# Kernel tuning notes

Hardware: AMD Instinct MI355X
Metric: run time of the kernel (lower is better)

The kernel has to match this reference:

```python
import jax, jax.numpy as jnp
import numpy as np

C = 64           # channels
CPG = 8          # channel_per_group
G = C // CPG     # offset groups = 8
K = 27           # 3x3x3 taps
N, D, H, W = 2, 8, 56, 56


def conv3d(x, w, b=None):
    y = jax.lax.conv_general_dilated(
        x, w, window_strides=(1, 1, 1), padding=[(1, 1)] * 3,
        dimension_numbers=('NCDHW', 'OIDHW', 'NCDHW'))
    if b is not None:
        y = y + b.reshape(1, -1, 1, 1, 1)
    return y


def deform_conv3d(x, off, w, groups):
    # x: [N,C,D,H,W]; off: [N, G*3*27, D,H,W]; w: [O,C,3,3,3]
    n, cin, d, h, wd = x.shape
    cpg = cin // groups
    p = d * h * wd
    off = off.reshape(n, groups, K, 3, d, h, wd)
    # kernel tap displacements in (kd,kh,kw) order, each in {-1,0,1}
    r = jnp.arange(3, dtype=x.dtype) - 1.0
    taps = jnp.stack(jnp.meshgrid(r, r, r, indexing='ij'), axis=-1).reshape(K, 3)
    gd = jnp.arange(d, dtype=x.dtype)[:, None, None]
    gh = jnp.arange(h, dtype=x.dtype)[None, :, None]
    gw = jnp.arange(wd, dtype=x.dtype)[None, None, :]
    # sampling positions [N,G,K,D,H,W]
    pd = gd + taps[:, 0][:, None, None, None] + off[:, :, :, 0]
    ph = gh + taps[:, 1][:, None, None, None] + off[:, :, :, 1]
    pw = gw + taps[:, 2][:, None, None, None] + off[:, :, :, 2]
    d0 = jnp.floor(pd); h0 = jnp.floor(ph); w0 = jnp.floor(pw)
    fd, fh, fw = pd - d0, ph - h0, pw - w0
    d0 = d0.astype(jnp.int32); h0 = h0.astype(jnp.int32); w0 = w0.astype(jnp.int32)
    xflat = x.reshape(n, groups, cpg, p)[:, :, None]  # [N,G,1,Cpg,P]
    acc = jnp.zeros((n, groups, K, cpg, p), x.dtype)
    for cd in (0, 1):
        for ch in (0, 1):
            for cw in (0, 1):
                idd, idh, idw = d0 + cd, h0 + ch, w0 + cw
                wgt = ((fd if cd else 1.0 - fd)
                       * (fh if ch else 1.0 - fh)
                       * (fw if cw else 1.0 - fw))
                valid = ((idd >= 0) & (idd < d) & (idh >= 0) & (idh < h)
                         & (idw >= 0) & (idw < wd)).astype(x.dtype)
                lin = ((jnp.clip(idd, 0, d - 1) * h + jnp.clip(idh, 0, h - 1)) * wd
                       + jnp.clip(idw, 0, wd - 1))
                g = jnp.take_along_axis(xflat, lin.reshape(n, groups, K, 1, p), axis=-1)
                acc = acc + g * (wgt * valid).reshape(n, groups, K, 1, p)
    # [N,G,K,Cpg,P] -> [N,K,C,P]
    vals = acc.transpose(0, 2, 1, 3, 4).reshape(n, K, cin, p)
    out = jnp.einsum('oik,nkip->nop', w.reshape(w.shape[0], cin, K), vals)
    return out.reshape(n, -1, d, h, wd)


def batchnorm(x, gamma, beta, eps=1e-5):
    m = x.mean((0, 2, 3, 4), keepdims=True)
    v = x.var((0, 2, 3, 4), keepdims=True)
    return (gamma.reshape(1, -1, 1, 1, 1) * (x - m) * jax.lax.rsqrt(v + eps)
            + beta.reshape(1, -1, 1, 1, 1))


def setup_inputs() -> dict:
    key = jax.random.key(0)
    ks = jax.random.split(key, 4)
    fan = C * K
    x = jax.random.normal(ks[0], (N, C, D, H, W), jnp.float32)
    w_off = jax.random.normal(ks[1], (G * 3 * K, C, 3, 3, 3), jnp.float32) * 0.01
    b_off = jnp.zeros((G * 3 * K,), jnp.float32)
    w1 = jax.random.normal(ks[2], (C, C, 3, 3, 3), jnp.float32) / np.sqrt(fan).astype(np.float32)
    w2 = jax.random.normal(ks[3], (C, C, 3, 3, 3), jnp.float32) / np.sqrt(fan).astype(np.float32)
    return dict(x=x, w_off=w_off, b_off=b_off, w1=w1,
                gamma1=jnp.ones((C,), jnp.float32), beta1=jnp.zeros((C,), jnp.float32),
                w2=w2, b2=jnp.zeros((C,), jnp.float32),
                gamma2=jnp.ones((C,), jnp.float32), beta2=jnp.zeros((C,), jnp.float32))


def reference(x, w_off, b_off, w1, gamma1, beta1, w2, b2, gamma2, beta2):
    residual = x
    off = conv3d(x, w_off, b_off)
    out = deform_conv3d(x, off, w1, G)
    out = jax.nn.relu(batchnorm(out, gamma1, beta1))
    out = conv3d(out, w2, b2)
    out = batchnorm(out, gamma2, beta2) + residual
    return jax.nn.relu(out)
```

## Files before the change

### kernel.cpp

```cpp
#include <hip/hip_runtime.h>
#include <hip/hip_bf16.h>

#define N_ 2
#define C_ 64
#define D_ 8
#define H_ 56
#define W_ 56
#define HW_ (H_*W_)
#define P_ (D_*HW_)
#define G_ 8
#define CPG_ 8
#define K_ 27
#define CO_OFF_ 648
#define MP_ 768
#define KK_ 1728
#define KB_ (KK_*2)

typedef __attribute__((ext_vector_type(8))) short shortx8;
typedef __attribute__((ext_vector_type(4))) float floatx4;
#define AS1 __attribute__((address_space(1)))
#define AS3 __attribute__((address_space(3)))

__device__ inline float b2f(unsigned short u) {
    union { unsigned u; float f; } x; x.u = ((unsigned)u) << 16; return x.f;
}
__device__ inline unsigned short f2b(float f) {
    union { float f; unsigned u; } x; x.f = f;
    unsigned r = (x.u + 0x7fffu + ((x.u >> 16) & 1u)) >> 16;
    return (unsigned short)r;
}
__device__ inline float lof(unsigned u) { union { unsigned u; float f; } x; x.u = u << 16; return x.f; }
__device__ inline float hif(unsigned u) { union { unsigned u; float f; } x; x.u = u & 0xffff0000u; return x.f; }


__global__ __launch_bounds__(256) void transpose_xt_kernel(
    const float* __restrict__ x, unsigned short* __restrict__ xt)
{
    __shared__ unsigned short tile[64][65];
    int b  = blockIdx.x;
    int n  = b / (P_/64);
    int p0 = (b % (P_/64))*64;
    int tid = threadIdx.x;
    int j  = tid & 63;
    int c0 = (tid >> 6)*16;
    for (int r = 0; r < 16; ++r)
        tile[c0 + r][j] = f2b(x[((size_t)n*C_ + c0 + r)*P_ + p0 + j]);
    __syncthreads();
    unsigned* dst = (unsigned*)(xt + ((size_t)n*P_ + p0)*C_);
    #pragma unroll
    for (int it = 0; it < 8; ++it) {
        int wi  = it*256 + tid;
        int row = wi >> 5;
        int c   = (wi & 31)*2;
        unsigned lo = tile[c][row], hi = tile[c+1][row];
        dst[(size_t)row*32 + (wi & 31)] = lo | (hi << 16);
    }
}

__global__ __launch_bounds__(256) void permA1k_kernel(
    const float* __restrict__ w, unsigned short* __restrict__ A)
{
    int i = blockIdx.x*256 + threadIdx.x;
    if (i >= MP_*KK_) return;
    int m = i / KK_, r = i % KK_;
    int kk = r / 64, ci = r % 64;
    A[i] = (m < CO_OFF_) ? f2b(w[((size_t)m*C_ + ci)*K_ + kk]) : (unsigned short)0;
}

__global__ __launch_bounds__(256) void perm_w_kernel(
    const float* __restrict__ w, unsigned short* __restrict__ At)
{
    int tid = blockIdx.x*256 + threadIdx.x;
    if (tid >= C_*KK_) return;
    int o  = tid / KK_;
    int r  = tid % KK_;
    int k  = r / 64, i = r % 64;
    At[tid] = f2b(w[((size_t)o*C_ + i)*K_ + k]);
}

__global__ __launch_bounds__(256) void conv_off_fused(
    const unsigned short* __restrict__ A,
    const unsigned short* __restrict__ xt,
    const float* __restrict__ bias,
    unsigned short* __restrict__ off2)
{
    __shared__ __align__(16) short As[2][16*512];
    __shared__ __align__(16) short Bs[16*512];
    int tid = threadIdx.x;
    int w = tid >> 6, lane = tid & 63;
    int n   = blockIdx.x / 980;
    int bid = blockIdx.x % 980;
    int mt, nt;
    if (bid < 960) { int c = bid/40, r = bid%40; mt = r >> 3; nt = c*8 + (r&7); }
    else           { int r = bid - 960;          mt = r >> 2; nt = 192 + (r&3); }
    int m0 = mt*128, p0 = nt*128;
    int lm = lane & 15, lq = lane >> 4;

    const unsigned short* xtn = xt + (size_t)n*P_*C_;
    unsigned short* out2 = off2 + (size_t)n*216*P_*3;

    const char* Ab0 = (const char*)A + (size_t)(m0 + w*32 + lm)*KB_ + lq*16;
    const char* Ab1 = Ab0 + (size_t)16*KB_;

    int oct = lane & 7;
    int prj[4], dj[4], hj[4], wj[4];
    #pragma unroll
    for (int j = 0; j < 4; ++j) {
        int prow = j*32 + w*8 + (lane >> 3);
        prj[j] = prow;
        int p = p0 + prow;
        dj[j] = p / HW_;
        int hw2 = p % HW_;
        hj[j] = hw2 / W_;
        wj[j] = hw2 % W_;
    }

    auto stageA = [&](int kt, int buf) {
        __builtin_amdgcn_global_load_lds((const AS1 unsigned*)(Ab0 + kt*128),      (AS3 unsigned*)(&As[buf][(w*2)*512]),     16, 0, 0);
        __builtin_amdgcn_global_load_lds((const AS1 unsigned*)(Ab1 + kt*128),      (AS3 unsigned*)(&As[buf][(w*2+1)*512]),   16, 0, 0);
        __builtin_amdgcn_global_load_lds((const AS1 unsigned*)(Ab0 + kt*128 + 64), (AS3 unsigned*)(&As[buf][(8+w*2)*512]),   16, 0, 0);
        __builtin_amdgcn_global_load_lds((const AS1 unsigned*)(Ab1 + kt*128 + 64), (AS3 unsigned*)(&As[buf][(8+w*2+1)*512]), 16, 0, 0);
    };
    auto loadB = [&](int kt, uint4* B) {
        int kd = kt/9 - 1, kh = (kt/3)%3 - 1, kw = kt%3 - 1;
        int delta = kd*HW_ + kh*W_ + kw;
        #pragma unroll
        for (int j = 0; j < 4; ++j) {
            bool v = ((unsigned)(dj[j]+kd) < (unsigned)D_) &&
                     ((unsigned)(hj[j]+kh) < (unsigned)H_) &&
                     ((unsigned)(wj[j]+kw) < (unsigned)W_);
            uint4 val = {0u,0u,0u,0u};
            if (v) val = *(const uint4*)(xtn + (size_t)(p0 + prj[j] + delta)*C_ + oct*8);
            B[j] = val;
        }
    };

    int mh = w >> 1, nh = w & 1;
    floatx4 acc[4][4];
    #pragma unroll
    for (int i = 0; i < 4; ++i)
        #pragma unroll
        for (int j = 0; j < 4; ++j)
            acc[i][j] = (floatx4){0.f, 0.f, 0.f, 0.f};

    uint4 Bcur[4], Bnext[4];
    #pragma unroll
    for (int j = 0; j < 4; ++j) Bnext[j] = (uint4){0u,0u,0u,0u};
    stageA(0, 0);
    loadB(0, Bcur);

    for (int kt = 0; kt < 27; ++kt) {
        int buf = kt & 1;
        __syncthreads();
        #pragma unroll
        for (int j = 0; j < 4; ++j) {
            int chunk = (oct>>2)*8 + (prj[j]>>4);
            *(uint4*)&Bs[chunk*512 + ((oct&3)*16 + ((prj[j]&15) ^ oct))*8] = Bcur[j];
        }
        __syncthreads();
        if (kt < 26) { stageA(kt+1, buf^1); loadB(kt+1, Bnext); }
        #pragma unroll
        for (int ks = 0; ks < 2; ++ks) {
            int swzB = (lq*16 + (lm ^ (ks*4 + lq)))*8;
            shortx8 a[4], b[4];
            #pragma unroll
            for (int i = 0; i < 4; ++i) a[i] = *(const shortx8*)&As[buf][(ks*8 + 4*mh + i)*512 + lane*8];
            #pragma unroll
            for (int j = 0; j < 4; ++j) b[j] = *(const shortx8*)&Bs[(ks*8 + 4*nh + j)*512 + swzB];
            #pragma unroll
            for (int i = 0; i < 4; ++i)
                #pragma unroll
                for (int j = 0; j < 4; ++j)
                    acc[i][j] = __builtin_amdgcn_mfma_f32_16x16x32_bf16(a[i], b[j], acc[i][j], 0, 0, 0);
        }
        #pragma unroll
        for (int j = 0; j < 4; ++j) Bcur[j] = Bnext[j];
    }

    #pragma unroll
    for (int i = 0; i < 4; ++i) {
        int cob = m0 + (4*mh+i)*16 + lq*4;
        #pragma unroll
        for (int r = 0; r < 4; ++r) {
            int co = cob + r;
            float bv = bias[co];
            int row2 = co / 3, comp = co % 3;
            size_t base = (size_t)row2*P_*3 + comp;
            #pragma unroll
            for (int j = 0; j < 4; ++j) {
                int col = p0 + (4*nh+j)*16 + lm;
                out2[base + (size_t)col*3] = f2b(acc[i][j][r] + bv);
            }
        }
    }
}

__global__ __launch_bounds__(256) void conv_off_tail(
    const unsigned short* __restrict__ A,
    const unsigned short* __restrict__ xt,
    const float* __restrict__ bias,
    unsigned short* __restrict__ off2)
{
    __shared__ __align__(16) short As[54*512];
    __shared__ __align__(16) short Bs[16*512];
    int tid = threadIdx.x;
    int w = tid >> 6, lane = tid & 63;
    int n  = blockIdx.x / 196;
    int p0 = (blockIdx.x % 196)*128;
    int lm = lane & 15, lq = lane >> 4;

    const unsigned short* xtn = xt + (size_t)n*P_*C_;
    unsigned short* out2 = off2 + (size_t)n*216*P_*3;

    const char* Abase = (const char*)A + (size_t)(640 + lm)*KB_ + lq*16;
    for (int ch = w; ch < 54; ch += 4)
        __builtin_amdgcn_global_load_lds((const AS1 unsigned*)(Abase + ch*64),
                                         (AS3 unsigned*)(As + ch*512), 16, 0, 0);

    int oct = lane & 7;
    int prj[4], dj[4], hj[4], wj[4];
    #pragma unroll
    for (int j = 0; j < 4; ++j) {
        int prow = j*32 + w*8 + (lane >> 3);
        prj[j] = prow;
        int p = p0 + prow;
        dj[j] = p / HW_;
        int hw2 = p % HW_;
        hj[j] = hw2 / W_;
        wj[j] = hw2 % W_;
    }
    auto loadB = [&](int kt, uint4* B) {
        int kd = kt/9 - 1, kh = (kt/3)%3 - 1, kw = kt%3 - 1;
        int delta = kd*HW_ + kh*W_ + kw;
        #pragma unroll
        for (int j = 0; j < 4; ++j) {
            bool v = ((unsigned)(dj[j]+kd) < (unsigned)D_) &&
                     ((unsigned)(hj[j]+kh) < (unsigned)H_) &&
                     ((unsigned)(wj[j]+kw) < (unsigned)W_);
            uint4 val = {0u,0u,0u,0u};
            if (v) val = *(const uint4*)(xtn + (size_t)(p0 + prj[j] + delta)*C_ + oct*8);
            B[j] = val;
        }
    };

    floatx4 acc[2];
    acc[0] = (floatx4){0.f,0.f,0.f,0.f};
    acc[1] = (floatx4){0.f,0.f,0.f,0.f};

    uint4 Bcur[4], Bnext[4];
    #pragma unroll
    for (int j = 0; j < 4; ++j) Bnext[j] = (uint4){0u,0u,0u,0u};
    loadB(0, Bcur);

    for (int kt = 0; kt < 27; ++kt) {
        __syncthreads();
        #pragma unroll
        for (int j = 0; j < 4; ++j) {
            int chunk = (oct>>2)*8 + (prj[j]>>4);
            *(uint4*)&Bs[chunk*512 + ((oct&3)*16 + ((prj[j]&15) ^ oct))*8] = Bcur[j];
        }
        __syncthreads();
        if (kt < 26) loadB(kt+1, Bnext);
        #pragma unroll
        for (int ks = 0; ks < 2; ++ks) {
            int swzB = (lq*16 + (lm ^ (ks*4 + lq)))*8;
            shortx8 a = *(const shortx8*)&As[(kt*2 + ks)*512 + lane*8];
            #pragma unroll
            for (int j = 0; j < 2; ++j) {
                shortx8 b = *(const shortx8*)&Bs[(ks*8 + w*2 + j)*512 + swzB];
                acc[j] = __builtin_amdgcn_mfma_f32_16x16x32_bf16(a, b, acc[j], 0, 0, 0);
            }
        }
        #pragma unroll
        for (int j = 0; j < 4; ++j) Bcur[j] = Bnext[j];
    }

    #pragma unroll
    for (int j = 0; j < 2; ++j) {
        #pragma unroll
        for (int r = 0; r < 4; ++r) {
            int co = 640 + lq*4 + r;
            if (co < CO_OFF_) {
                int col = p0 + w*32 + j*16 + lm;
                out2[((size_t)(co/3)*P_ + col)*3 + (co%3)] = f2b(acc[j][r] + bias[co]);
            }
        }
    }
}

__global__ __launch_bounds__(256) void deform_fused(
    const unsigned short* __restrict__ xt,
    const unsigned short* __restrict__ off2,
    const unsigned short* __restrict__ A,
    unsigned short* __restrict__ y1t)
{
    __shared__ __align__(16) short SH[12288];
    int tid = threadIdx.x;
    int w = tid >> 6, lane = tid & 63;
    int n  = blockIdx.x / (P_/32);
    int p0 = (blockIdx.x % (P_/32))*32;
    int lm = lane & 15, lq = lane >> 4;

    const unsigned short* offn = off2 + (size_t)n*216*P_*3;
    const uint4* xg0 = (const uint4*)(xt + (size_t)n*P_*C_);

    const char* Ab = (const char*)A + (size_t)(w*16 + lm)*KB_ + lq*16;

    int g = lane & 7;
    int prow = tid >> 3;
    int p = p0 + prow;
    int dd = p / HW_;
    int hw2 = p % HW_;
    int hh = hw2 / W_;
    int ww = hw2 % W_;
    int bchunk = (g>>2)*2 + (prow>>4);
    int boffs  = ((g&3)*16 + ((prow&15) ^ g))*8;

    auto stageA = [&](int kt, int buf) {
        __builtin_amdgcn_global_load_lds((const AS1 unsigned*)(Ab + kt*128),      (AS3 unsigned*)(SH + buf*4096 + w*512),     16, 0, 0);
        __builtin_amdgcn_global_load_lds((const AS1 unsigned*)(Ab + kt*128 + 64), (AS3 unsigned*)(SH + buf*4096 + (4+w)*512), 16, 0, 0);
    };
    auto loadOff = [&](int kt, float* o) {
        size_t idx = ((size_t)(g*K_ + kt)*P_ + p)*3;
        o[0] = b2f(offn[idx]);
        o[1] = b2f(offn[idx + 1]);
        o[2] = b2f(offn[idx + 2]);
    };
    auto issueCorners = [&](int kt, float* o, uint4* V, float* Wt) {
        int kd = kt/9 - 1, kh = (kt/3)%3 - 1, kw = kt%3 - 1;
        float pd = (float)(dd + kd) + o[0];
        float ph = (float)(hh + kh) + o[1];
        float pw = (float)(ww + kw) + o[2];
        float fd0 = floorf(pd), fh0 = floorf(ph), fw0 = floorf(pw);
        int d0 = (int)fd0, h0 = (int)fh0, w0i = (int)fw0;
        float fd = pd - fd0, fh = ph - fh0, fw = pw - fw0;
        int dc0 = min(max(d0, 0), D_-1),   dc1 = min(max(d0+1, 0), D_-1);
        int hc0 = min(max(h0, 0), H_-1),   hc1 = min(max(h0+1, 0), H_-1);
        int wc0 = min(max(w0i, 0), W_-1),  wc1 = min(max(w0i+1, 0), W_-1);
        float wd0 = ((unsigned)d0      < (unsigned)D_) ? 1.f - fd : 0.f;
        float wd1 = ((unsigned)(d0+1)  < (unsigned)D_) ? fd       : 0.f;
        float wh0 = ((unsigned)h0      < (unsigned)H_) ? 1.f - fh : 0.f;
        float wh1 = ((unsigned)(h0+1)  < (unsigned)H_) ? fh       : 0.f;
        float ww0 = ((unsigned)w0i     < (unsigned)W_) ? 1.f - fw : 0.f;
        float ww1 = ((unsigned)(w0i+1) < (unsigned)W_) ? fw       : 0.f;
        int rb00 = (dc0*H_ + hc0)*W_, rb01 = (dc0*H_ + hc1)*W_;
        int rb10 = (dc1*H_ + hc0)*W_, rb11 = (dc1*H_ + hc1)*W_;
        float wdh00 = wd0*wh0, wdh01 = wd0*wh1, wdh10 = wd1*wh0, wdh11 = wd1*wh1;
        V[0] = xg0[(size_t)(rb00+wc0)*8 + g];  Wt[0] = wdh00*ww0;
        V[1] = xg0[(size_t)(rb00+wc1)*8 + g];  Wt[1] = wdh00*ww1;
        V[2] = xg0[(size_t)(rb01+wc0)*8 + g];  Wt[2] = wdh01*ww0;
        V[3] = xg0[(size_t)(rb01+wc1)*8 + g];  Wt[3] = wdh01*ww1;
        V[4] = xg0[(size_t)(rb10+wc0)*8 + g];  Wt[4] = wdh10*ww0;
        V[5] = xg0[(size_t)(rb10+wc1)*8 + g];  Wt[5] = wdh10*ww1;
        V[6] = xg0[(size_t)(rb11+wc0)*8 + g];  Wt[6] = wdh11*ww0;
        V[7] = xg0[(size_t)(rb11+wc1)*8 + g];  Wt[7] = wdh11*ww1;
    };
    auto reduceCorners = [&](uint4* V, float* Wt, uint4& o4) {
        float res[CPG_];
        #pragma unroll
        for (int c = 0; c < CPG_; ++c) res[c] = 0.f;
        #pragma unroll
        for (int c = 0; c < 8; ++c) {
            uint4 v4 = V[c];
            float wgt = Wt[c];
            res[0] = fmaf(wgt, lof(v4.x), res[0]);
            res[1] = fmaf(wgt, hif(v4.x), res[1]);
            res[2] = fmaf(wgt, lof(v4.y), res[2]);
            res[3] = fmaf(wgt, hif(v4.y), res[3]);
            res[4] = fmaf(wgt, lof(v4.z), res[4]);
            res[5] = fmaf(wgt, hif(v4.z), res[5]);
            res[6] = fmaf(wgt, lof(v4.w), res[6]);
            res[7] = fmaf(wgt, hif(v4.w), res[7]);
        }
        o4.x = (unsigned)f2b(res[0]) | ((unsigned)f2b(res[1]) << 16);
        o4.y = (unsigned)f2b(res[2]) | ((unsigned)f2b(res[3]) << 16);
        o4.z = (unsigned)f2b(res[4]) | ((unsigned)f2b(res[5]) << 16);
        o4.w = (unsigned)f2b(res[6]) | ((unsigned)f2b(res[7]) << 16);
    };

    int mh = w >> 1, nh = w & 1;
    floatx4 acc[2];
    acc[0] = (floatx4){0.f,0.f,0.f,0.f};
    acc[1] = (floatx4){0.f,0.f,0.f,0.f};

    float offA[3], offB[3], offT[3];
    uint4 Vv[8]; float Wt[8];
    uint4 o4cur;

    stageA(0, 0);
    loadOff(0, offA);
    loadOff(1, offB);
    issueCorners(0, offA, Vv, Wt);
    reduceCorners(Vv, Wt, o4cur);
    *(uint4*)&SH[8192 + bchunk*512 + boffs] = o4cur;

    for (int kt = 0; kt < 27; ++kt) {
        int buf = kt & 1;
        __syncthreads();
        if (kt < 26) {
            stageA(kt+1, buf^1);
            if (kt < 25) loadOff(kt+2, offT);
            issueCorners(kt+1, offB, Vv, Wt);
        }
        #pragma unroll
        for (int ks = 0; ks < 2; ++ks) {
            int swzB = (lq*16 + (lm ^ (ks*4 + lq)))*8;
            shortx8 b = *(const shortx8*)&SH[8192 + buf*2048 + (ks*2 + nh)*512 + swzB];
            #pragma unroll
            for (int i = 0; i < 2; ++i) {
                shortx8 a = *(const shortx8*)&SH[buf*4096 + (ks*4 + 2*mh+i)*512 + lane*8];
                acc[i] = __builtin_amdgcn_mfma_f32_16x16x32_bf16(a, b, acc[i], 0, 0, 0);
            }
        }
        if (kt < 26) {
            reduceCorners(Vv, Wt, o4cur);
            *(uint4*)&SH[8192 + (buf^1)*2048 + bchunk*512 + boffs] = o4cur;
            offB[0] = offT[0]; offB[1] = offT[1]; offB[2] = offT[2];
        }
    }

    __syncthreads();
    #pragma unroll
    for (int i = 0; i < 2; ++i) {
        int ob = mh*32 + i*16 + lq*4;
        int pc = nh*16 + lm;
        #pragma unroll
        for (int rr = 0; rr < 4; ++rr)
            SH[pc*72 + ob + rr] = (short)f2b(acc[i][rr]);
    }
    __syncthreads();
    {
        int row = tid >> 3, seg = tid & 7;
        uint4 v = *(const uint4*)&SH[row*72 + seg*8];
        *(uint4*)(y1t + ((size_t)n*P_ + p0 + row)*C_ + seg*8) = v;
    }
}

__global__ __launch_bounds__(256) void conv2_fused(
    const unsigned short* __restrict__ y1t,
    const float* __restrict__ st1,
    const unsigned short* __restrict__ A,
    const float* __restrict__ bias,
    unsigned short* __restrict__ y2)
{
    __shared__ __align__(16) short As[2][4096];
    __shared__ float sc[64], sf[64];
    int tid = threadIdx.x;
    if (tid < 64) sc[tid] = st1[tid];
    else if (tid < 128) sf[tid-64] = st1[tid];
    int w = tid >> 6, lane = tid & 63;
    int n  = blockIdx.x / (P_/64);
    int p0 = (blockIdx.x % (P_/64))*64;
    int lm = lane & 15, lq = lane >> 4;

    const unsigned short* y1n = y1t + (size_t)n*P_*C_;
    unsigned short* y2n = y2 + (size_t)n*C_*P_;
    const char* Ab = (const char*)A + (size_t)(w*16 + lm)*KB_ + lq*16;

    int p = p0 + w*16 + lm;
    int dd = p / HW_, hw2 = p % HW_;
    int hh = hw2 / W_, ww = hw2 % W_;

    auto stageA = [&](int kt, int buf) {
        __builtin_amdgcn_global_load_lds((const AS1 unsigned*)(Ab + kt*128),      (AS3 unsigned*)(&As[buf][w*512]),     16, 0, 0);
        __builtin_amdgcn_global_load_lds((const AS1 unsigned*)(Ab + kt*128 + 64), (AS3 unsigned*)(&As[buf][(4+w)*512]), 16, 0, 0);
    };
    auto issueV = [&](int kt, uint4* V, int& M) {
        int kd = kt/9 - 1, kh = (kt/3)%3 - 1, kw = kt%3 - 1;
        int delta = kd*HW_ + kh*W_ + kw;
        bool v = ((unsigned)(dd+kd) < (unsigned)D_) &&
                 ((unsigned)(hh+kh) < (unsigned)H_) &&
                 ((unsigned)(ww+kw) < (unsigned)W_);
        M = v ? 1 : 0;
        #pragma unroll
        for (int ks = 0; ks < 2; ++ks) {
            uint4 val = {0u,0u,0u,0u};
            if (v) val = *(const uint4*)(y1n + (size_t)(p + delta)*C_ + (ks*4 + lq)*8);
            V[ks] = val;
        }
    };
    auto reduceT = [&](uint4 V, int ks, int M) -> shortx8 {
        uint4 o4 = {0u,0u,0u,0u};
        if (M) {
            int cb = (ks*4 + lq)*8;
            float r0 = fmaxf(lof(V.x)*sc[cb+0] + sf[cb+0], 0.f);
            float r1 = fmaxf(hif(V.x)*sc[cb+1] + sf[cb+1], 0.f);
            float r2 = fmaxf(lof(V.y)*sc[cb+2] + sf[cb+2], 0.f);
            float r3 = fmaxf(hif(V.y)*sc[cb+3] + sf[cb+3], 0.f);
            float r4 = fmaxf(lof(V.z)*sc[cb+4] + sf[cb+4], 0.f);
            float r5 = fmaxf(hif(V.z)*sc[cb+5] + sf[cb+5], 0.f);
            float r6 = fmaxf(lof(V.w)*sc[cb+6] + sf[cb+6], 0.f);
            float r7 = fmaxf(hif(V.w)*sc[cb+7] + sf[cb+7], 0.f);
            o4.x = (unsigned)f2b(r0) | ((unsigned)f2b(r1) << 16);
            o4.y = (unsigned)f2b(r2) | ((unsigned)f2b(r3) << 16);
            o4.z = (unsigned)f2b(r4) | ((unsigned)f2b(r5) << 16);
            o4.w = (unsigned)f2b(r6) | ((unsigned)f2b(r7) << 16);
        }
        return *(shortx8*)&o4;
    };

    floatx4 acc[4];
    #pragma unroll
    for (int i = 0; i < 4; ++i) acc[i] = (floatx4){0.f,0.f,0.f,0.f};

    uint4 V[2];
    int M;
    stageA(0, 0);
    issueV(0, V, M);

    for (int kt = 0; kt < 27; ++kt) {
        int buf = kt & 1;
        __syncthreads();
        if (kt < 26) stageA(kt+1, buf^1);
        shortx8 b0 = reduceT(V[0], 0, M);
        shortx8 b1 = reduceT(V[1], 1, M);
        if (kt < 26) issueV(kt+1, V, M);
        #pragma unroll
        for (int i = 0; i < 4; ++i) {
            shortx8 a = *(const shortx8*)&As[buf][(0*4 + i)*512 + lane*8];
            acc[i] = __builtin_amdgcn_mfma_f32_16x16x32_bf16(a, b0, acc[i], 0, 0, 0);
        }
        #pragma unroll
        for (int i = 0; i < 4; ++i) {
            shortx8 a = *(const shortx8*)&As[buf][(1*4 + i)*512 + lane*8];
            acc[i] = __builtin_amdgcn_mfma_f32_16x16x32_bf16(a, b1, acc[i], 0, 0, 0);
        }
    }

    #pragma unroll
    for (int i = 0; i < 4; ++i) {
        #pragma unroll
        for (int r = 0; r < 4; ++r) {
            int co = i*16 + lq*4 + r;
            y2n[(size_t)co*P_ + p] = f2b(acc[i][r] + bias[co]);
        }
    }
}

__global__ __launch_bounds__(256) void stats_partial_kernel(
    const unsigned short* __restrict__ y1t, float* __restrict__ part)
{
    int b = blockIdx.x, tid = threadIdx.x;
    int c = tid & 63, sub = tid >> 6;
    float s = 0.f, q = 0.f;
    for (int rr = 0; rr < 128; ++rr) {
        int row = b*512 + sub*128 + rr;
        float v = b2f(y1t[(size_t)row*C_ + c]);
        s += v;
        q = fmaf(v, v, q);
    }
    __shared__ float ss[256], qq[256];
    ss[tid] = s; qq[tid] = q;
    __syncthreads();
    if (tid < 64) {
        float S = ss[tid] + ss[64+tid] + ss[128+tid] + ss[192+tid];
        float Q = qq[tid] + qq[64+tid] + qq[128+tid] + qq[192+tid];
        part[b*128 + tid]      = S;
        part[b*128 + 64 + tid] = Q;
    }
}

__global__ void stats_final_kernel(
    const float* __restrict__ part,
    const float* __restrict__ gamma, const float* __restrict__ beta,
    float* __restrict__ st1)
{
    int c = threadIdx.x;
    float S = 0.f, Q = 0.f;
    for (int b = 0; b < 98; ++b) {
        S += part[b*128 + c];
        Q += part[b*128 + 64 + c];
    }
    const float inv = 1.f / (float)(N_*P_);
    float m = S * inv;
    float var = Q * inv - m*m;
    float scale = rsqrtf(var + 1e-5f) * gamma[c];
    st1[c]      = scale;
    st1[64 + c] = beta[c] - m*scale;
}

__global__ __launch_bounds__(256) void bn_stats_kernel(
    const unsigned short* __restrict__ src, float* __restrict__ stats)
{
    int c   = blockIdx.x;
    int tid = threadIdx.x;
    float s = 0.f, q = 0.f;
    for (int n = 0; n < N_; ++n) {
        const unsigned short* p = src + ((size_t)n*C_ + c)*P_;
        for (int i = tid; i < P_; i += 256) {
            float v = b2f(p[i]);
            s += v;
            q = fmaf(v, v, q);
        }
    }
    #pragma unroll
    for (int o = 32; o; o >>= 1) {
        s += __shfl_down(s, o);
        q += __shfl_down(q, o);
    }
    __shared__ float sh[2][4];
    int wave = tid >> 6;
    if ((tid & 63) == 0) { sh[0][wave] = s; sh[1][wave] = q; }
    __syncthreads();
    if (tid == 0) {
        float S = sh[0][0] + sh[0][1] + sh[0][2] + sh[0][3];
        float Q = sh[1][0] + sh[1][1] + sh[1][2] + sh[1][3];
        const float inv = 1.f / (float)(N_*P_);
        float m  = S * inv;
        float var = Q * inv - m*m;
        stats[c]      = m;
        stats[C_ + c] = rsqrtf(var + 1e-5f);
    }
}

__global__ __launch_bounds__(256) void bn_add_relu_kernel(
    const unsigned short* __restrict__ y2, const float* __restrict__ x,
    const float* __restrict__ stats,
    const float* __restrict__ gamma, const float* __restrict__ beta,
    float* __restrict__ out)
{
    size_t idx = (size_t)blockIdx.x*256 + threadIdx.x;
    int c = (int)((idx / P_) % C_);
    float v = (b2f(y2[idx]) - stats[c]) * stats[C_ + c] * gamma[c] + beta[c] + x[idx];
    out[idx] = fmaxf(v, 0.f);
}

extern "C" void kernel_launch(void* const* d_in, const int* in_sizes, int n_in,
                              void* d_out, int out_size, void* d_ws, size_t ws_size,
                              hipStream_t stream) {
    const float* x     = (const float*)d_in[0];
    const float* w_off = (const float*)d_in[1];
    const float* b_off = (const float*)d_in[2];
    const float* w1    = (const float*)d_in[3];
    const float* g1    = (const float*)d_in[4];
    const float* be1   = (const float*)d_in[5];
    const float* w2    = (const float*)d_in[6];
    const float* b2    = (const float*)d_in[7];
    const float* g2    = (const float*)d_in[8];
    const float* be2   = (const float*)d_in[9];
    float* out = (float*)d_out;

    float* st1  = (float*)d_ws;
    float* st2  = st1 + 128;
    float* part = st2 + 128;
    unsigned short* off2 = (unsigned short*)(part + 98*128);
    unsigned short* xt  = off2 + (size_t)N_*216*P_*3;
    unsigned short* y1t = xt  + (size_t)N_*P_*C_;
    unsigned short* y2  = y1t + (size_t)N_*P_*C_;
    unsigned short* A1k = y2  + (size_t)N_*C_*P_;
    unsigned short* A1t = A1k + (size_t)MP_*KK_;
    unsigned short* A2t = A1t + (size_t)C_*KK_;

    transpose_xt_kernel<<<N_*(P_/64), 256, 0, stream>>>(x, xt);
    permA1k_kernel<<<(MP_*KK_+255)/256, 256, 0, stream>>>(w_off, A1k);
    perm_w_kernel<<<(C_*KK_+255)/256, 256, 0, stream>>>(w1, A1t);
    perm_w_kernel<<<(C_*KK_+255)/256, 256, 0, stream>>>(w2, A2t);

    conv_off_fused<<<2*980, 256, 0, stream>>>(A1k, xt, b_off, off2);
    conv_off_tail<<<2*196, 256, 0, stream>>>(A1k, xt, b_off, off2);

    deform_fused<<<N_*(P_/32), 256, 0, stream>>>(xt, off2, A1t, y1t);

    stats_partial_kernel<<<98, 256, 0, stream>>>(y1t, part);
    stats_final_kernel<<<1, 64, 0, stream>>>(part, g1, be1, st1);

    conv2_fused<<<N_*(P_/64), 256, 0, stream>>>(y1t, st1, A2t, b2, y2);

    bn_stats_kernel<<<C_, 256, 0, stream>>>(y2, st2);
    bn_add_relu_kernel<<<(N_*C_*P_)/256, 256, 0, stream>>>(y2, x, st2, g2, be2, out);
}
```

Measured before the change: 542.3 us.

## Deepen deformable gather pipeline with two corner buffers and packed bf16 converts

Restructures the deformable-conv main loop into a two-tap unrolled schedule with separate corner register sets, so the gathers for tap k+2 are in flight while tap k+1 is reduced and tap k is multiplied. Offsets are prefetched further ahead. The trilinear weights are factored into six values instead of eight, and index arithmetic is moved to 32-bit unsigned. Manual bf16 rounding is replaced by the hardware v_cvt_pk_bf16_f32 instruction in both the deform and conv2 kernels. This raises register pressure, which may lower occupancy.

Result: no change. 538.1 us (-0.8%).

```diff
diff --git a/kernel.cpp b/kernel.cpp
--- a/kernel.cpp
+++ b/kernel.cpp
@@ -31,6 +31,11 @@
 }
 __device__ inline float lof(unsigned u) { union { unsigned u; float f; } x; x.u = u << 16; return x.f; }
 __device__ inline float hif(unsigned u) { union { unsigned u; float f; } x; x.u = u & 0xffff0000u; return x.f; }
+__device__ inline unsigned cvt_pk_bf16(float a, float b) {
+    unsigned r;
+    asm("v_cvt_pk_bf16_f32 %0, %1, %2" : "=v"(r) : "v"(a), "v"(b));
+    return r;
+}
 
 
 __global__ __launch_bounds__(256) void transpose_xt_kernel(
@@ -314,19 +319,19 @@
     int hh = hw2 / W_;
     int ww = hw2 % W_;
     int bchunk = (g>>2)*2 + (prow>>4);
-    int boffs  = ((g&3)*16 + ((prow&15) ^ g))*8;
+    int bsoff  = bchunk*512 + ((g&3)*16 + ((prow&15) ^ g))*8;
+
+    const unsigned short* offp = offn + ((size_t)(g*K_)*P_ + p)*3;
 
     auto stageA = [&](int kt, int buf) {
         __builtin_amdgcn_global_load_lds((const AS1 unsigned*)(Ab + kt*128),      (AS3 unsigned*)(SH + buf*4096 + w*512),     16, 0, 0);
         __builtin_amdgcn_global_load_lds((const AS1 unsigned*)(Ab + kt*128 + 64), (AS3 unsigned*)(SH + buf*4096 + (4+w)*512), 16, 0, 0);
     };
     auto loadOff = [&](int kt, float* o) {
-        size_t idx = ((size_t)(g*K_ + kt)*P_ + p)*3;
-        o[0] = b2f(offn[idx]);
-        o[1] = b2f(offn[idx + 1]);
-        o[2] = b2f(offn[idx + 2]);
-    };
-    auto issueCorners = [&](int kt, float* o, uint4* V, float* Wt) {
+        const unsigned short* q = offp + (unsigned)(kt*(P_*3));
+        o[0] = b2f(q[0]); o[1] = b2f(q[1]); o[2] = b2f(q[2]);
+    };
+    auto issueCorners = [&](int kt, const float* o, uint4* V, float* Wt) {
         int kd = kt/9 - 1, kh = (kt/3)%3 - 1, kw = kt%3 - 1;
         float pd = (float)(dd + kd) + o[0];
         float ph = (float)(hh + kh) + o[1];
@@ -341,28 +346,31 @@
         float wd1 = ((unsigned)(d0+1)  < (unsigned)D_) ? fd       : 0.f;
         float wh0 = ((unsigned)h0      < (unsigned)H_) ? 1.f - fh : 0.f;
         float wh1 = ((unsigned)(h0+1)  < (unsigned)H_) ? fh       : 0.f;
-        float ww0 = ((unsigned)w0i     < (unsigned)W_) ? 1.f - fw : 0.f;
-        float ww1 = ((unsigned)(w0i+1) < (unsigned)W_) ? fw       : 0.f;
-        int rb00 = (dc0*H_ + hc0)*W_, rb01 = (dc0*H_ + hc1)*W_;
-        int rb10 = (dc1*H_ + hc0)*W_, rb11 = (dc1*H_ + hc1)*W_;
-        float wdh00 = wd0*wh0, wdh01 = wd0*wh1, wdh10 = wd1*wh0, wdh11 = wd1*wh1;
-        V[0] = xg0[(size_t)(rb00+wc0)*8 + g];  Wt[0] = wdh00*ww0;
-        V[1] = xg0[(size_t)(rb00+wc1)*8 + g];  Wt[1] = wdh00*ww1;
-        V[2] = xg0[(size_t)(rb01+wc0)*8 + g];  Wt[2] = wdh01*ww0;
-        V[3] = xg0[(size_t)(rb01+wc1)*8 + g];  Wt[3] = wdh01*ww1;
-        V[4] = xg0[(size_t)(rb10+wc0)*8 + g];  Wt[4] = wdh10*ww0;
-        V[5] = xg0[(size_t)(rb10+wc1)*8 + g];  Wt[5] = wdh10*ww1;
-        V[6] = xg0[(size_t)(rb11+wc0)*8 + g];  Wt[6] = wdh11*ww0;
-        V[7] = xg0[(size_t)(rb11+wc1)*8 + g];  Wt[7] = wdh11*ww1;
-    };
-    auto reduceCorners = [&](uint4* V, float* Wt, uint4& o4) {
-        float res[CPG_];
-        #pragma unroll
-        for (int c = 0; c < CPG_; ++c) res[c] = 0.f;
+        Wt[4] = ((unsigned)w0i     < (unsigned)W_) ? 1.f - fw : 0.f;
+        Wt[5] = ((unsigned)(w0i+1) < (unsigned)W_) ? fw       : 0.f;
+        Wt[0] = wd0*wh0; Wt[1] = wd0*wh1; Wt[2] = wd1*wh0; Wt[3] = wd1*wh1;
+        unsigned rb00 = (unsigned)((dc0*H_ + hc0)*W_)*8u + (unsigned)g;
+        unsigned rb01 = (unsigned)((dc0*H_ + hc1)*W_)*8u + (unsigned)g;
+        unsigned rb10 = (unsigned)((dc1*H_ + hc0)*W_)*8u + (unsigned)g;
+        unsigned rb11 = (unsigned)((dc1*H_ + hc1)*W_)*8u + (unsigned)g;
+        unsigned c0 = (unsigned)wc0*8u, c1 = (unsigned)wc1*8u;
+        V[0] = xg0[rb00 + c0];
+        V[1] = xg0[rb00 + c1];
+        V[2] = xg0[rb01 + c0];
+        V[3] = xg0[rb01 + c1];
+        V[4] = xg0[rb10 + c0];
+        V[5] = xg0[rb10 + c1];
+        V[6] = xg0[rb11 + c0];
+        V[7] = xg0[rb11 + c1];
+    };
+    auto reduceStore = [&](const uint4* V, const float* Wt, int half) {
+        float res[8];
+        #pragma unroll
+        for (int c = 0; c < 8; ++c) res[c] = 0.f;
         #pragma unroll
         for (int c = 0; c < 8; ++c) {
             uint4 v4 = V[c];
-            float wgt = Wt[c];
+            float wgt = Wt[c>>1] * ((c & 1) ? Wt[5] : Wt[4]);
             res[0] = fmaf(wgt, lof(v4.x), res[0]);
             res[1] = fmaf(wgt, hif(v4.x), res[1]);
             res[2] = fmaf(wgt, lof(v4.y), res[2]);
@@ -372,10 +380,12 @@
             res[6] = fmaf(wgt, lof(v4.w), res[6]);
             res[7] = fmaf(wgt, hif(v4.w), res[7]);
         }
-        o4.x = (unsigned)f2b(res[0]) | ((unsigned)f2b(res[1]) << 16);
-        o4.y = (unsigned)f2b(res[2]) | ((unsigned)f2b(res[3]) << 16);
-        o4.z = (unsigned)f2b(res[4]) | ((unsigned)f2b(res[5]) << 16);
-        o4.w = (unsigned)f2b(res[6]) | ((unsigned)f2b(res[7]) << 16);
+        uint4 o4;
+        o4.x = cvt_pk_bf16(res[0], res[1]);
+        o4.y = cvt_pk_bf16(res[2], res[3]);
+        o4.z = cvt_pk_bf16(res[4], res[5]);
+        o4.w = cvt_pk_bf16(res[6], res[7]);
+        *(uint4*)&SH[8192 + half*2048 + bsoff] = o4;
     };
 
     int mh = w >> 1, nh = w & 1;
@@ -383,25 +393,7 @@
     acc[0] = (floatx4){0.f,0.f,0.f,0.f};
     acc[1] = (floatx4){0.f,0.f,0.f,0.f};
 
-    float offA[3], offB[3], offT[3];
-    uint4 Vv[8]; float Wt[8];
-    uint4 o4cur;
-
-    stageA(0, 0);
-    loadOff(0, offA);
-    loadOff(1, offB);
-    issueCorners(0, offA, Vv, Wt);
-    reduceCorners(Vv, Wt, o4cur);
-    *(uint4*)&SH[8192 + bchunk*512 + boffs] = o4cur;
-
-    for (int kt = 0; kt < 27; ++kt) {
-        int buf = kt & 1;
-        __syncthreads();
-        if (kt < 26) {
-            stageA(kt+1, buf^1);
-            if (kt < 25) loadOff(kt+2, offT);
-            issueCorners(kt+1, offB, Vv, Wt);
-        }
+    auto doMFMA = [&](int buf) {
         #pragma unroll
         for (int ks = 0; ks < 2; ++ks) {
             int swzB = (lq*16 + (lm ^ (ks*4 + lq)))*8;
@@ -412,12 +404,41 @@
                 acc[i] = __builtin_amdgcn_mfma_f32_16x16x32_bf16(a, b, acc[i], 0, 0, 0);
             }
         }
-        if (kt < 26) {
-            reduceCorners(Vv, Wt, o4cur);
-            *(uint4*)&SH[8192 + (buf^1)*2048 + bchunk*512 + boffs] = o4cur;
-            offB[0] = offT[0]; offB[1] = offT[1]; offB[2] = offT[2];
-        }
-    }
+    };
+
+    uint4 VA[8], VB[8];
+    float WA[6], WB[6];
+    float oC[3], oD[3], oE[3], oF[3];
+
+    stageA(0, 0);
+    {
+        float o0[3], o1[3];
+        loadOff(0, o0); loadOff(1, o1); loadOff(2, oC); loadOff(3, oD);
+        issueCorners(0, o0, VA, WA);
+        issueCorners(1, o1, VB, WB);
+        reduceStore(VA, WA, 0);
+    }
+
+    for (int kt = 0; kt < 26; kt += 2) {
+        __syncthreads();
+        stageA(kt+1, 1);
+        issueCorners(kt+2, oC, VA, WA);
+        if (kt+4 <= 26) loadOff(kt+4, oE);
+        doMFMA(0);
+        reduceStore(VB, WB, 1);
+
+        __syncthreads();
+        stageA(kt+2, 0);
+        if (kt+3 <= 26) issueCorners(kt+3, oD, VB, WB);
+        if (kt+5 <= 26) loadOff(kt+5, oF);
+        doMFMA(1);
+        reduceStore(VA, WA, 0);
+
+        oC[0]=oE[0]; oC[1]=oE[1]; oC[2]=oE[2];
+        oD[0]=oF[0]; oD[1]=oF[1]; oD[2]=oF[2];
+    }
+    __syncthreads();
+    doMFMA(0);
 
     __syncthreads();
     #pragma unroll
@@ -491,10 +512,10 @@
             float r5 = fmaxf(hif(V.z)*sc[cb+5] + sf[cb+5], 0.f);
             float r6 = fmaxf(lof(V.w)*sc[cb+6] + sf[cb+6], 0.f);
             float r7 = fmaxf(hif(V.w)*sc[cb+7] + sf[cb+7], 0.f);
-            o4.x = (unsigned)f2b(r0) | ((unsigned)f2b(r1) << 16);
-            o4.y = (unsigned)f2b(r2) | ((unsigned)f2b(r3) << 16);
-            o4.z = (unsigned)f2b(r4) | ((unsigned)f2b(r5) << 16);
-            o4.w = (unsigned)f2b(r6) | ((unsigned)f2b(r7) << 16);
+            o4.x = cvt_pk_bf16(r0, r1);
+            o4.y = cvt_pk_bf16(r2, r3);
+            o4.z = cvt_pk_bf16(r4, r5);
+            o4.w = cvt_pk_bf16(r6, r7);
         }
         return *(shortx8*)&o4;
     };
```

## Widen offset-conv GEMM tile to 256 columns and use packed bf16 convert

Applied to the files above, without the earlier changes.

The offset convolution GEMM tile grows from 128x128 to 128x256 output positions per block. This halves the grid, doubles the per-wave accumulator count and reuses each A fragment across eight B fragments, cutting repeated A-operand loads from LDS and global memory. In exchange, register pressure and LDS usage rise, the launch bounds now ask for two blocks per CU, and the old L2-friendly tile ordering is dropped in favour of a plain mt/nt split. Separately, the manual bf16 rounding in the deform and conv2 kernels is replaced by the hardware v_cvt_pk_bf16_f32 instruction.

Result: faster. 516.7 us (-4.7%).

```diff
diff --git a/kernel.cpp b/kernel.cpp
--- a/kernel.cpp
+++ b/kernel.cpp
@@ -31,6 +31,11 @@
 }
 __device__ inline float lof(unsigned u) { union { unsigned u; float f; } x; x.u = u << 16; return x.f; }
 __device__ inline float hif(unsigned u) { union { unsigned u; float f; } x; x.u = u & 0xffff0000u; return x.f; }
+__device__ inline unsigned cvt_pk_bf16(float a, float b) {
+    unsigned r;
+    asm("v_cvt_pk_bf16_f32 %0, %1, %2" : "=v"(r) : "v"(a), "v"(b));
+    return r;
+}
 
 
 __global__ __launch_bounds__(256) void transpose_xt_kernel(
@@ -78,22 +83,20 @@
     At[tid] = f2b(w[((size_t)o*C_ + i)*K_ + k]);
 }
 
-__global__ __launch_bounds__(256) void conv_off_fused(
+__global__ __launch_bounds__(256, 2) void conv_off_fused(
     const unsigned short* __restrict__ A,
     const unsigned short* __restrict__ xt,
     const float* __restrict__ bias,
     unsigned short* __restrict__ off2)
 {
     __shared__ __align__(16) short As[2][16*512];
-    __shared__ __align__(16) short Bs[16*512];
+    __shared__ __align__(16) short Bs[32*512];
     int tid = threadIdx.x;
     int w = tid >> 6, lane = tid & 63;
-    int n   = blockIdx.x / 980;
-    int bid = blockIdx.x % 980;
-    int mt, nt;
-    if (bid < 960) { int c = bid/40, r = bid%40; mt = r >> 3; nt = c*8 + (r&7); }
-    else           { int r = bid - 960;          mt = r >> 2; nt = 192 + (r&3); }
-    int m0 = mt*128, p0 = nt*128;
+    int n   = blockIdx.x / 490;
+    int bid = blockIdx.x % 490;
+    int mt = bid / 98, nt = bid % 98;
+    int m0 = mt*128, p0 = nt*256;
     int lm = lane & 15, lq = lane >> 4;
 
     const unsigned short* xtn = xt + (size_t)n*P_*C_;
@@ -103,9 +106,9 @@
     const char* Ab1 = Ab0 + (size_t)16*KB_;
 
     int oct = lane & 7;
-    int prj[4], dj[4], hj[4], wj[4];
-    #pragma unroll
-    for (int j = 0; j < 4; ++j) {
+    int prj[8], dj[8], hj[8], wj[8];
+    #pragma unroll
+    for (int j = 0; j < 8; ++j) {
         int prow = j*32 + w*8 + (lane >> 3);
         prj[j] = prow;
         int p = p0 + prow;
@@ -125,7 +128,7 @@
         int kd = kt/9 - 1, kh = (kt/3)%3 - 1, kw = kt%3 - 1;
         int delta = kd*HW_ + kh*W_ + kw;
         #pragma unroll
-        for (int j = 0; j < 4; ++j) {
+        for (int j = 0; j < 8; ++j) {
             bool v = ((unsigned)(dj[j]+kd) < (unsigned)D_) &&
                      ((unsigned)(hj[j]+kh) < (unsigned)H_) &&
                      ((unsigned)(wj[j]+kw) < (unsigned)W_);
@@ -136,16 +139,16 @@
     };
 
     int mh = w >> 1, nh = w & 1;
-    floatx4 acc[4][4];
+    floatx4 acc[4][8];
     #pragma unroll
     for (int i = 0; i < 4; ++i)
         #pragma unroll
-        for (int j = 0; j < 4; ++j)
+        for (int j = 0; j < 8; ++j)
             acc[i][j] = (floatx4){0.f, 0.f, 0.f, 0.f};
 
-    uint4 Bcur[4], Bnext[4];
-    #pragma unroll
-    for (int j = 0; j < 4; ++j) Bnext[j] = (uint4){0u,0u,0u,0u};
+    uint4 Bcur[8], Bnext[8];
+    #pragma unroll
+    for (int j = 0; j < 8; ++j) Bnext[j] = (uint4){0u,0u,0u,0u};
     stageA(0, 0);
     loadB(0, Bcur);
 
@@ -153,8 +156,8 @@
         int buf = kt & 1;
         __syncthreads();
         #pragma unroll
-        for (int j = 0; j < 4; ++j) {
-            int chunk = (oct>>2)*8 + (prj[j]>>4);
+        for (int j = 0; j < 8; ++j) {
+            int chunk = (oct>>2)*16 + (prj[j]>>4);
             *(uint4*)&Bs[chunk*512 + ((oct&3)*16 + ((prj[j]&15) ^ oct))*8] = Bcur[j];
         }
         __syncthreads();
@@ -162,19 +165,19 @@
         #pragma unroll
         for (int ks = 0; ks < 2; ++ks) {
             int swzB = (lq*16 + (lm ^ (ks*4 + lq)))*8;
-            shortx8 a[4], b[4];
+            shortx8 a[4];
             #pragma unroll
             for (int i = 0; i < 4; ++i) a[i] = *(const shortx8*)&As[buf][(ks*8 + 4*mh + i)*512 + lane*8];
             #pragma unroll
-            for (int j = 0; j < 4; ++j) b[j] = *(const shortx8*)&Bs[(ks*8 + 4*nh + j)*512 + swzB];
-            #pragma unroll
-            for (int i = 0; i < 4; ++i)
+            for (int j = 0; j < 8; ++j) {
+                shortx8 b = *(const shortx8*)&Bs[(ks*16 + 8*nh + j)*512 + swzB];
                 #pragma unroll
-                for (int j = 0; j < 4; ++j)
-                    acc[i][j] = __builtin_amdgcn_mfma_f32_16x16x32_bf16(a[i], b[j], acc[i][j], 0, 0, 0);
-        }
-        #pragma unroll
-        for (int j = 0; j < 4; ++j) Bcur[j] = Bnext[j];
+                for (int i = 0; i < 4; ++i)
+                    acc[i][j] = __builtin_amdgcn_mfma_f32_16x16x32_bf16(a[i], b, acc[i][j], 0, 0, 0);
+            }
+        }
+        #pragma unroll
+        for (int j = 0; j < 8; ++j) Bcur[j] = Bnext[j];
     }
 
     #pragma unroll
@@ -187,8 +190,8 @@
             int row2 = co / 3, comp = co % 3;
             size_t base = (size_t)row2*P_*3 + comp;
             #pragma unroll
-            for (int j = 0; j < 4; ++j) {
-                int col = p0 + (4*nh+j)*16 + lm;
+            for (int j = 0; j < 8; ++j) {
+                int col = p0 + (8*nh+j)*16 + lm;
                 out2[base + (size_t)col*3] = f2b(acc[i][j][r] + bv);
             }
         }
@@ -372,10 +375,10 @@
             res[6] = fmaf(wgt, lof(v4.w), res[6]);
             res[7] = fmaf(wgt, hif(v4.w), res[7]);
         }
-        o4.x = (unsigned)f2b(res[0]) | ((unsigned)f2b(res[1]) << 16);
-        o4.y = (unsigned)f2b(res[2]) | ((unsigned)f2b(res[3]) << 16);
-        o4.z = (unsigned)f2b(res[4]) | ((unsigned)f2b(res[5]) << 16);
-        o4.w = (unsigned)f2b(res[6]) | ((unsigned)f2b(res[7]) << 16);
+        o4.x = cvt_pk_bf16(res[0], res[1]);
+        o4.y = cvt_pk_bf16(res[2], res[3]);
+        o4.z = cvt_pk_bf16(res[4], res[5]);
+        o4.w = cvt_pk_bf16(res[6], res[7]);
     };
 
     int mh = w >> 1, nh = w & 1;
@@ -491,10 +494,10 @@
             float r5 = fmaxf(hif(V.z)*sc[cb+5] + sf[cb+5], 0.f);
             float r6 = fmaxf(lof(V.w)*sc[cb+6] + sf[cb+6], 0.f);
             float r7 = fmaxf(hif(V.w)*sc[cb+7] + sf[cb+7], 0.f);
-            o4.x = (unsigned)f2b(r0) | ((unsigned)f2b(r1) << 16);
-            o4.y = (unsigned)f2b(r2) | ((unsigned)f2b(r3) << 16);
-            o4.z = (unsigned)f2b(r4) | ((unsigned)f2b(r5) << 16);
-            o4.w = (unsigned)f2b(r6) | ((unsigned)f2b(r7) << 16);
+            o4.x = cvt_pk_bf16(r0, r1);
+            o4.y = cvt_pk_bf16(r2, r3);
+            o4.z = cvt_pk_bf16(r4, r5);
+            o4.w = cvt_pk_bf16(r6, r7);
         }
         return *(shortx8*)&o4;
     };
@@ -656,7 +659,7 @@
     perm_w_kernel<<<(C_*KK_+255)/256, 256, 0, stream>>>(w1, A1t);
     perm_w_kernel<<<(C_*KK_+255)/256, 256, 0, stream>>>(w2, A2t);
 
-    conv_off_fused<<<2*980, 256, 0, stream>>>(A1k, xt, b_off, off2);
+    conv_off_fused<<<2*490, 256, 0, stream>>>(A1k, xt, b_off, off2);
     conv_off_tail<<<2*196, 256, 0, stream>>>(A1k, xt, b_off, off2);
 
     deform_fused<<<N_*(P_/32), 256, 0, stream>>>(xt, off2, A1t, y1t);
```
